# Performance work log

Hardware: AMD Instinct MI355X
Metric: run time of the kernel (lower is better)

## Reference

```python
import jax, jax.numpy as jnp
import numpy as np

N = 256          # batch size
C = 100          # nb_classes
D = 512          # sz_embed
SCALE = 3.0
EPS = 1e-12      # F.normalize eps
M = N * (N - 1) // 2  # number of (i<j) candidate pairs


def l2norm(x):
    # matches F.normalize(p=2, dim=-1) with eps=1e-12
    return x / jnp.maximum(jnp.linalg.norm(x, axis=-1, keepdims=True), EPS)


def dist_block(A, B):
    # squared euclidean distance block of pairwise_distance(cat([A,B]))[0][:len(A), len(A):]
    # (off-diagonal block, so the eye-masking in the original is a no-op; negatives zeroed)
    d = (A * A).sum(-1, keepdims=True) + (B * B).sum(-1)[None, :] - 2.0 * (A @ B.T)
    return jnp.maximum(d, 0.0)


def setup_inputs() -> dict:
    key = jax.random.key(0)
    k1, k2, k3 = jax.random.split(key, 3)
    X = jax.random.normal(k1, (N, D), dtype=jnp.float32)
    proxies = jax.random.normal(k2, (C, D), dtype=jnp.float32) / 8.0
    T = jax.random.randint(k3, (N,), 0, C)
    indices = jnp.arange(N)  # unused by forward, kept for signature fidelity
    return {"X": X, "proxies": proxies, "T": T, "indices": indices}


def reference(X, proxies, T, indices):
    Pn = SCALE * l2norm(proxies)           # (C, D)
    Xn = SCALE * l2norm(X)                 # (N, D)
    IP = Xn @ Pn.T                         # (N, C) inner-product block

    # --- intercls_mixup (method=1, uncertainty-guided lambdas) ---
    # all i<j pairs; same-class pairs are masked out (original skips them in a Python loop)
    i1, i2 = jnp.triu_indices(N, k=1)      # (M,), (M,)
    diff = T[i1] != T[i2]                  # (M,) valid cross-class pairs
    c1, c2 = T[i1], T[i2]

    X1P1 = jnp.clip(IP[i1, c1], -1.0, 1.0)
    X1P2 = jnp.clip(IP[i1, c2], -1.0, 1.0)
    X2P1 = jnp.clip(IP[i2, c1], -1.0, 1.0)
    X2P2 = jnp.clip(IP[i2, c2], -1.0, 1.0)
    lam = jnp.clip((X2P2 - X2P1) / (X2P2 - X2P1 + X1P1 - X1P2), 0.3, 0.7)
    lam = jnp.where(diff, lam, 0.5)        # neutralize masked (same-class) pairs

    virt = lam[:, None] * Xn[i1] + (1.0 - lam[:, None]) * Xn[i2]  # (M, D)
    virt = l2norm(virt)

    # --- proxy-NCA loss over real + virtual samples ---
    Xall = jnp.concatenate([Xn, SCALE * virt], axis=0)            # (N+M, D)
    Dall = dist_block(Xall, Pn)                                   # (N+M, C)
    logsm = jax.nn.log_softmax(-Dall, axis=-1)

    loss_real = -logsm[jnp.arange(N), T]                          # one-hot targets
    lv = logsm[N:]                                                # (M, C)
    rows = jnp.arange(M)
    # virtual soft targets: lam*onehot(c1) + (1-lam)*onehot(c2)
    loss_virt = -(lam * lv[rows, c1] + (1.0 - lam) * lv[rows, c2])

    total = loss_real.sum() + jnp.sum(jnp.where(diff, loss_virt, 0.0))
    count = N + diff.sum()
    return total / count
```

## Files before the change

kernel.cpp:

```cpp
#include <hip/hip_runtime.h>
#include <hip/hip_bf16.h>
#include <math.h>

#define N_ 256
#define C_ 100
#define D_ 512
#define ST 368
#define NTILE 23
#define NWTILE 529
#define LOG2E 1.44269504088896f

typedef __attribute__((ext_vector_type(8))) short short8;
typedef __attribute__((ext_vector_type(4))) float floatx4;

__device__ inline float waveReduceSum(float v) {
    #pragma unroll
    for (int off = 32; off > 0; off >>= 1) v += __shfl_xor(v, off, 64);
    return v;
}
__device__ inline float clip1(float x) { return fminf(fmaxf(x, -1.0f), 1.0f); }

__device__ inline short8 cvt8(float4 a, float4 b) {
    union { __hip_bfloat16 h[8]; short8 s; } u;
    u.h[0] = __float2bfloat16(a.x); u.h[1] = __float2bfloat16(a.y);
    u.h[2] = __float2bfloat16(a.z); u.h[3] = __float2bfloat16(a.w);
    u.h[4] = __float2bfloat16(b.x); u.h[5] = __float2bfloat16(b.y);
    u.h[6] = __float2bfloat16(b.z); u.h[7] = __float2bfloat16(b.w);
    return u.s;
}

__global__ void gemm_kernel(const float* __restrict__ X,
                            const float* __restrict__ P,
                            float* __restrict__ G,
                            float* __restrict__ rn) {
    int wid = blockIdx.x * 4 + (threadIdx.x >> 6);
    if (wid >= NWTILE) return;
    int lane = threadIdx.x & 63;
    int r = lane & 15, quad = lane >> 4;
    int tm = wid / NTILE, tn = wid - tm * NTILE;
    int ra = tm * 16 + r; if (ra >= 356) ra = 0;
    int rb = tn * 16 + r; if (rb >= 356) rb = 0;
    const float* arow = (ra < N_) ? (X + (size_t)ra * D_) : (P + (size_t)(ra - N_) * D_);
    const float* brow = (rb < N_) ? (X + (size_t)rb * D_) : (P + (size_t)(rb - N_) * D_);
    floatx4 acc = {0.0f, 0.0f, 0.0f, 0.0f};
    #pragma unroll
    for (int kc = 0; kc < D_; kc += 32) {
        const float4* ap = (const float4*)(arow + kc + quad * 8);
        const float4* bp = (const float4*)(brow + kc + quad * 8);
        short8 av = cvt8(ap[0], ap[1]);
        short8 bv = cvt8(bp[0], bp[1]);
        acc = __builtin_amdgcn_mfma_f32_16x16x32_bf16(av, bv, acc, 0, 0, 0);
    }
    int row0 = tm * 16 + quad * 4, col = tn * 16 + r;
    #pragma unroll
    for (int i = 0; i < 4; ++i)
        G[(size_t)(row0 + i) * ST + col] = acc[i];
    if (tm == tn && (r >> 2) == quad) {
        float d = acc[r & 3];
        rn[tm * 16 + r] = 3.0f * rsqrtf(fmaxf(d, 1e-24f));
    }
}

__global__ __launch_bounds__(512)
void pair_real_kernel(const float* __restrict__ G,
                      const float* __restrict__ rn,
                      const int* __restrict__ T,
                      float* __restrict__ out) {
    __shared__ int hist[C_];
    __shared__ float s2[8], ssum[8];
    int t = threadIdx.x;
    int w = t >> 6, lane = t & 63;

    if (t < C_) hist[t] = 0;
    __syncthreads();
    if (t < N_) atomicAdd(&hist[T[t]], 1);
    __syncthreads();
    float same = 0.0f;
    if (t < C_) { float n = (float)hist[t]; same = 0.5f * n * (n - 1.0f); }
    float rs = waveReduceSum(same);
    if (lane == 0) s2[w] = rs;
    __syncthreads();
    float cnt = 256.0f + 32640.0f;
    #pragma unroll
    for (int k = 0; k < 8; ++k) cnt -= s2[k];

    int i1 = blockIdx.x;
    int i2 = t >> 1;
    int p  = t & 1;
    bool diag = (i2 == i1);
    int t1 = T[i1], t2 = T[i2];
    bool act = diag || ((i2 > i1) && (t2 != t1));
    const float* sp = rn + 256;
    float contrib = 0.0f;

    if (__ballot(act)) {
        if (act) {
            float s1 = rn[i1], sc2 = rn[i2];
            const float* row1 = G + (size_t)i1 * ST + 256;
            const float* row2 = G + (size_t)i2 * ST + 256;
            float ip1t1 = row1[t1] * s1 * sp[t1];
            float ip1t2 = row1[t2] * s1 * sp[t2];
            float ip2t1 = row2[t1] * sc2 * sp[t1];
            float ip2t2 = row2[t2] * sc2 * sp[t2];
            float X1P1 = clip1(ip1t1), X1P2 = clip1(ip1t2);
            float X2P1 = clip1(ip2t1), X2P2 = clip1(ip2t2);
            float num = X2P2 - X2P1;
            float den = num + X1P1 - X1P2;
            float lam = fminf(fmaxf(num / den, 0.3f), 0.7f);
            if (diag) lam = 1.0f;
            float oml = 1.0f - lam;
            float g = G[(size_t)i1 * ST + i2] * s1 * sc2;
            float wn2 = 9.0f * (lam * lam + oml * oml) + 2.0f * lam * oml * g;
            float ss2 = 6.0f * rsqrtf(fmaxf(wn2, 1e-24f));
            float la = ss2 * lam * s1 * LOG2E, lb = ss2 * oml * sc2 * LOG2E;
            float sm0 = 0.0f, sm1 = 0.0f, sm2 = 0.0f, sm3 = 0.0f;
            #pragma unroll 4
            for (int c = 4 * p; c < C_; c += 8) {
                float4 a1 = *(const float4*)(row1 + c);
                float4 a2 = *(const float4*)(row2 + c);
                float4 s4 = *(const float4*)(sp + c);
                sm0 += exp2f(s4.x * (la * a1.x + lb * a2.x));
                sm1 += exp2f(s4.y * (la * a1.y + lb * a2.y));
                sm2 += exp2f(s4.z * (la * a1.z + lb * a2.z));
                sm3 += exp2f(s4.w * (la * a1.w + lb * a2.w));
            }
            float sm = (sm0 + sm1) + (sm2 + sm3);
            sm += __shfl_xor(sm, 1, 64);
            if (p == 0) {
                float LSE = logf(sm);
                float ec1 = ss2 * (lam * ip1t1 + oml * ip2t1);
                float ec2 = ss2 * (lam * ip1t2 + oml * ip2t2);
                contrib = LSE - lam * ec1 - oml * ec2;
            }
        }
    }
    contrib = waveReduceSum(contrib);
    if (lane == 0) ssum[w] = contrib;
    __syncthreads();
    if (t == 0) {
        float bs = 0.0f;
        #pragma unroll
        for (int k = 0; k < 8; ++k) bs += ssum[k];
        atomicAdd(out, bs / cnt);
    }
}

extern "C" void kernel_launch(void* const* d_in, const int* in_sizes, int n_in,
                              void* d_out, int out_size, void* d_ws, size_t ws_size,
                              hipStream_t stream) {
    const float* X = (const float*)d_in[0];
    const float* P = (const float*)d_in[1];
    const int*   T = (const int*)d_in[2];
    float* ws = (float*)d_ws;
    float* G  = ws;
    float* rn = ws + 135424;
    float* out = (float*)d_out;

    gemm_kernel<<<133, 256, 0, stream>>>(X, P, G, rn);
    pair_real_kernel<<<N_, 512, 0, stream>>>(G, rn, T, out);
}
```

Baseline: 73.42 us.

## Fuse GEMM and pair-loss into single kernel with per-block LDS proxy slab

Replaces the separate GEMM and pair-loss kernels with one fused kernel. Each block converts the proxies to bf16 in LDS, computes inner products for its 129 circularly-indexed rows with MFMA, and evaluates the pair losses directly from LDS. This removes the global intermediate and one launch and balances pairs across blocks. The cost is redundant proxy conversion and GEMM work in every block, and large LDS use that limits occupancy to one block per CU.

Measured after the change: 83.69 us. +14.0%, slower.

```diff
diff --git a/kernel.cpp b/kernel.cpp
--- a/kernel.cpp
+++ b/kernel.cpp
@@ -5,10 +5,19 @@
 #define N_ 256
 #define C_ 100
 #define D_ 512
-#define ST 368
-#define NTILE 23
-#define NWTILE 529
 #define LOG2E 1.44269504088896f
+#define XPST 102
+#define PBROWB 64
+#define PBSLAB 6464
+
+#define OFF_PB    0
+#define OFF_XPN   103424
+#define OFF_TL    156056
+#define OFF_HIST  157080
+#define OFF_SPS   157480
+#define OFF_RED   157928
+#define OFF_S2    157960
+#define LDS_TOTAL 157992
 
 typedef __attribute__((ext_vector_type(8))) short short8;
 typedef __attribute__((ext_vector_type(4))) float floatx4;
@@ -29,119 +38,171 @@
     return u.s;
 }
 
-__global__ void gemm_kernel(const float* __restrict__ X,
-                            const float* __restrict__ P,
-                            float* __restrict__ G,
-                            float* __restrict__ rn) {
-    int wid = blockIdx.x * 4 + (threadIdx.x >> 6);
-    if (wid >= NWTILE) return;
-    int lane = threadIdx.x & 63;
-    int r = lane & 15, quad = lane >> 4;
-    int tm = wid / NTILE, tn = wid - tm * NTILE;
-    int ra = tm * 16 + r; if (ra >= 356) ra = 0;
-    int rb = tn * 16 + r; if (rb >= 356) rb = 0;
-    const float* arow = (ra < N_) ? (X + (size_t)ra * D_) : (P + (size_t)(ra - N_) * D_);
-    const float* brow = (rb < N_) ? (X + (size_t)rb * D_) : (P + (size_t)(rb - N_) * D_);
-    floatx4 acc = {0.0f, 0.0f, 0.0f, 0.0f};
-    #pragma unroll
-    for (int kc = 0; kc < D_; kc += 32) {
-        const float4* ap = (const float4*)(arow + kc + quad * 8);
-        const float4* bp = (const float4*)(brow + kc + quad * 8);
-        short8 av = cvt8(ap[0], ap[1]);
-        short8 bv = cvt8(bp[0], bp[1]);
-        acc = __builtin_amdgcn_mfma_f32_16x16x32_bf16(av, bv, acc, 0, 0, 0);
-    }
-    int row0 = tm * 16 + quad * 4, col = tn * 16 + r;
-    #pragma unroll
-    for (int i = 0; i < 4; ++i)
-        G[(size_t)(row0 + i) * ST + col] = acc[i];
-    if (tm == tn && (r >> 2) == quad) {
-        float d = acc[r & 3];
-        rn[tm * 16 + r] = 3.0f * rsqrtf(fmaxf(d, 1e-24f));
-    }
-}
-
 __global__ __launch_bounds__(512)
-void pair_real_kernel(const float* __restrict__ G,
-                      const float* __restrict__ rn,
-                      const int* __restrict__ T,
-                      float* __restrict__ out) {
-    __shared__ int hist[C_];
-    __shared__ float s2[8], ssum[8];
+void fused_kernel(const float* __restrict__ X, const float* __restrict__ P,
+                  const int* __restrict__ T, float* __restrict__ out) {
+    extern __shared__ char smem[];
+    short* Pb   = (short*)(smem + OFF_PB);
+    float* XPn  = (float*)(smem + OFF_XPN);
+    int*   Tl   = (int*)(smem + OFF_TL);
+    int*   hist = (int*)(smem + OFF_HIST);
+    float* sps  = (float*)(smem + OFF_SPS);
+    float* red  = (float*)(smem + OFF_RED);
+    float* s2   = (float*)(smem + OFF_S2);
+
     int t = threadIdx.x;
     int w = t >> 6, lane = t & 63;
+    int b = blockIdx.x;
 
     if (t < C_) hist[t] = 0;
+    if (t < N_) Tl[t] = T[t];
+
+    for (int j = 0; j < 13; ++j) {
+        int ch = t + 512 * j;
+        float s8 = 0.0f;
+        if (ch < 6400) {
+            int pr = ch >> 6, cl = ch & 63;
+            const float4* pp = (const float4*)(P + (size_t)pr * D_ + cl * 8);
+            float4 a = pp[0], c4 = pp[1];
+            s8 = a.x*a.x + a.y*a.y + a.z*a.z + a.w*a.w
+               + c4.x*c4.x + c4.y*c4.y + c4.z*c4.z + c4.w*c4.w;
+            short8 v = cvt8(a, c4);
+            *(short8*)((char*)Pb + (cl >> 2) * PBSLAB + pr * PBROWB + (cl & 3) * 16) = v;
+        }
+        float rs = waveReduceSum(s8);
+        int pr0 = w + 8 * j;
+        if (lane == 0 && pr0 < C_) sps[pr0] = 3.0f * rsqrtf(fmaxf(rs, 1e-24f));
+    }
+    if (t < 64) {
+        const float4* xp = (const float4*)(X + (size_t)b * D_ + t * 8);
+        short8 v = cvt8(xp[0], xp[1]);
+        *(short8*)((char*)Pb + (t >> 2) * PBSLAB + 100 * PBROWB + (t & 3) * 16) = v;
+    }
+    float sxb;
+    {
+        const float4* xp = (const float4*)(X + (size_t)b * D_ + lane * 8);
+        float4 a = xp[0], c4 = xp[1];
+        float xb2 = a.x*a.x + a.y*a.y + a.z*a.z + a.w*a.w
+                  + c4.x*c4.x + c4.y*c4.y + c4.z*c4.z + c4.w*c4.w;
+        xb2 = waveReduceSum(xb2);
+        sxb = 3.0f * rsqrtf(fmaxf(xb2, 1e-24f));
+    }
+
     __syncthreads();
-    if (t < N_) atomicAdd(&hist[T[t]], 1);
+
+    if (t < N_) atomicAdd(&hist[Tl[t]], 1);
+
+    int r = lane & 15, quad = lane >> 4;
+    int boff[7];
+    #pragma unroll
+    for (int tn = 0; tn < 7; ++tn) {
+        int cb = tn * 16 + r;
+        if (cb > 100) cb = 0;
+        boff[tn] = cb * PBROWB + quad * 16;
+    }
+    for (int rt = w; rt < 9; rt += 8) {
+        int lr0 = rt * 16;
+        int ra = (b + lr0 + r) & 255;
+        const float* arow = X + (size_t)ra * D_;
+        floatx4 acc[7];
+        #pragma unroll
+        for (int tn = 0; tn < 7; ++tn) acc[tn] = (floatx4){0.f, 0.f, 0.f, 0.f};
+        float nrm = 0.0f;
+        #pragma unroll 4
+        for (int kc = 0; kc < D_; kc += 32) {
+            const float4* ap = (const float4*)(arow + kc + quad * 8);
+            float4 a0 = ap[0], a1 = ap[1];
+            nrm += a0.x*a0.x + a0.y*a0.y + a0.z*a0.z + a0.w*a0.w
+                 + a1.x*a1.x + a1.y*a1.y + a1.z*a1.z + a1.w*a1.w;
+            short8 av = cvt8(a0, a1);
+            const char* sl = (const char*)Pb + (kc >> 5) * PBSLAB;
+            #pragma unroll
+            for (int tn = 0; tn < 7; ++tn) {
+                short8 bv = *(const short8*)(sl + boff[tn]);
+                acc[tn] = __builtin_amdgcn_mfma_f32_16x16x32_bf16(av, bv, acc[tn], 0, 0, 0);
+            }
+        }
+        nrm += __shfl_xor(nrm, 16, 64);
+        nrm += __shfl_xor(nrm, 32, 64);
+        float sxa = 3.0f * rsqrtf(fmaxf(nrm, 1e-24f));
+        float sxr[4];
+        #pragma unroll
+        for (int i = 0; i < 4; ++i) sxr[i] = __shfl(sxa, quad * 4 + i, 64);
+        #pragma unroll
+        for (int tn = 0; tn < 7; ++tn) {
+            int colw = tn * 16 + r;
+            if (colw <= 100) {
+                float cs = (colw < 100) ? sps[colw] : sxb;
+                #pragma unroll
+                for (int i = 0; i < 4; ++i) {
+                    int lr = lr0 + quad * 4 + i;
+                    if (lr <= 128) XPn[lr * XPST + colw] = acc[tn][i] * sxr[i] * cs;
+                }
+            }
+        }
+    }
     __syncthreads();
+
     float same = 0.0f;
     if (t < C_) { float n = (float)hist[t]; same = 0.5f * n * (n - 1.0f); }
-    float rs = waveReduceSum(same);
-    if (lane == 0) s2[w] = rs;
-    __syncthreads();
-    float cnt = 256.0f + 32640.0f;
-    #pragma unroll
-    for (int k = 0; k < 8; ++k) cnt -= s2[k];
-
-    int i1 = blockIdx.x;
-    int i2 = t >> 1;
-    int p  = t & 1;
-    bool diag = (i2 == i1);
-    int t1 = T[i1], t2 = T[i2];
-    bool act = diag || ((i2 > i1) && (t2 != t1));
-    const float* sp = rn + 256;
+    float rsame = waveReduceSum(same);
+    if (lane == 0) s2[w] = rsame;
+
+    int m = t >> 1, p = t & 1;
+    bool diag = (m == 128);
+    int d = m + 1;
+    int lr2 = diag ? 0 : d;
+    int i2 = diag ? b : ((b + d) & 255);
+    bool isPair = (m < 127) || (m == 127 && b < 128);
+    int t1 = Tl[b], t2 = Tl[i2];
+    bool act = diag || (isPair && (t2 != t1));
     float contrib = 0.0f;
-
     if (__ballot(act)) {
         if (act) {
-            float s1 = rn[i1], sc2 = rn[i2];
-            const float* row1 = G + (size_t)i1 * ST + 256;
-            const float* row2 = G + (size_t)i2 * ST + 256;
-            float ip1t1 = row1[t1] * s1 * sp[t1];
-            float ip1t2 = row1[t2] * s1 * sp[t2];
-            float ip2t1 = row2[t1] * sc2 * sp[t1];
-            float ip2t2 = row2[t2] * sc2 * sp[t2];
-            float X1P1 = clip1(ip1t1), X1P2 = clip1(ip1t2);
-            float X2P1 = clip1(ip2t1), X2P2 = clip1(ip2t2);
+            const float* rowA = XPn;
+            const float* rowB = XPn + lr2 * XPST;
+            float ip11 = rowA[t1], ip12 = rowA[t2];
+            float ip21 = rowB[t1], ip22 = rowB[t2];
+            float X1P1 = clip1(ip11), X1P2 = clip1(ip12);
+            float X2P1 = clip1(ip21), X2P2 = clip1(ip22);
             float num = X2P2 - X2P1;
             float den = num + X1P1 - X1P2;
             float lam = fminf(fmaxf(num / den, 0.3f), 0.7f);
             if (diag) lam = 1.0f;
             float oml = 1.0f - lam;
-            float g = G[(size_t)i1 * ST + i2] * s1 * sc2;
+            float g = rowB[100];
             float wn2 = 9.0f * (lam * lam + oml * oml) + 2.0f * lam * oml * g;
             float ss2 = 6.0f * rsqrtf(fmaxf(wn2, 1e-24f));
-            float la = ss2 * lam * s1 * LOG2E, lb = ss2 * oml * sc2 * LOG2E;
-            float sm0 = 0.0f, sm1 = 0.0f, sm2 = 0.0f, sm3 = 0.0f;
+            float la = ss2 * lam * LOG2E, lb = ss2 * oml * LOG2E;
+            float sm0 = 0, sm1 = 0, sm2 = 0, sm3 = 0;
             #pragma unroll 4
-            for (int c = 4 * p; c < C_; c += 8) {
-                float4 a1 = *(const float4*)(row1 + c);
-                float4 a2 = *(const float4*)(row2 + c);
-                float4 s4 = *(const float4*)(sp + c);
-                sm0 += exp2f(s4.x * (la * a1.x + lb * a2.x));
-                sm1 += exp2f(s4.y * (la * a1.y + lb * a2.y));
-                sm2 += exp2f(s4.z * (la * a1.z + lb * a2.z));
-                sm3 += exp2f(s4.w * (la * a1.w + lb * a2.w));
+            for (int k = 0; k < 13; ++k) {
+                int c = 4 * p + 8 * k;
+                if (c < C_) {
+                    sm0 += exp2f(la * rowA[c]     + lb * rowB[c]);
+                    sm1 += exp2f(la * rowA[c + 1] + lb * rowB[c + 1]);
+                    sm2 += exp2f(la * rowA[c + 2] + lb * rowB[c + 2]);
+                    sm3 += exp2f(la * rowA[c + 3] + lb * rowB[c + 3]);
+                }
             }
             float sm = (sm0 + sm1) + (sm2 + sm3);
             sm += __shfl_xor(sm, 1, 64);
             if (p == 0) {
                 float LSE = logf(sm);
-                float ec1 = ss2 * (lam * ip1t1 + oml * ip2t1);
-                float ec2 = ss2 * (lam * ip1t2 + oml * ip2t2);
+                float ec1 = ss2 * (lam * ip11 + oml * ip21);
+                float ec2 = ss2 * (lam * ip12 + oml * ip22);
                 contrib = LSE - lam * ec1 - oml * ec2;
             }
         }
     }
     contrib = waveReduceSum(contrib);
-    if (lane == 0) ssum[w] = contrib;
+    if (lane == 0) red[w] = contrib;
     __syncthreads();
     if (t == 0) {
-        float bs = 0.0f;
-        #pragma unroll
-        for (int k = 0; k < 8; ++k) bs += ssum[k];
-        atomicAdd(out, bs / cnt);
+        float bs = 0.0f, sc = 0.0f;
+        #pragma unroll
+        for (int k = 0; k < 8; ++k) { bs += red[k]; sc += s2[k]; }
+        atomicAdd(out, bs / (32896.0f - sc));
     }
 }
 
@@ -151,11 +212,13 @@
     const float* X = (const float*)d_in[0];
     const float* P = (const float*)d_in[1];
     const int*   T = (const int*)d_in[2];
-    float* ws = (float*)d_ws;
-    float* G  = ws;
-    float* rn = ws + 135424;
     float* out = (float*)d_out;
 
-    gemm_kernel<<<133, 256, 0, stream>>>(X, P, G, rn);
-    pair_real_kernel<<<N_, 512, 0, stream>>>(G, rn, T, out);
-}
+    static bool init = false;
+    if (!init) {
+        hipFuncSetAttribute((const void*)fused_kernel,
+                            hipFuncAttributeMaxDynamicSharedMemorySize, LDS_TOTAL);
+        init = true;
+    }
+    fused_kernel<<<N_, 512, LDS_TOTAL, stream>>>(X, P, T, out);
+}
```

## Rebalance pair kernel with circulant pairing and shared-memory staged rows

Applied to the files above, without the earlier changes.

Replaces the triangular per-row pair assignment (row i1 handles i2>i1, so block work is badly imbalanced) with a circulant scheme: each of 512 blocks handles row b paired with 64 cyclic offsets, giving every block equal work. The G rows for the partner samples, proxy scales, norms and labels are staged into LDS so the logsumexp loop reads shared memory, and 8 lanes split each pair's 100 classes. The histogram-based pair count is folded into the final reduction. The cost is extra LDS staging per block and more complex index logic for the half-offset (dd==128) case.

Result: slower. 77.54 us (+5.6%).

```diff
diff --git a/kernel.cpp b/kernel.cpp
--- a/kernel.cpp
+++ b/kernel.cpp
@@ -62,86 +62,104 @@
 }
 
 __global__ __launch_bounds__(512)
-void pair_real_kernel(const float* __restrict__ G,
-                      const float* __restrict__ rn,
-                      const int* __restrict__ T,
-                      float* __restrict__ out) {
-    __shared__ int hist[C_];
-    __shared__ float s2[8], ssum[8];
+void pair_kernel(const float* __restrict__ G, const float* __restrict__ rn,
+                 const int* __restrict__ T, float* __restrict__ out) {
+    __shared__ __attribute__((aligned(16))) float XPl[64 * 104];
+    __shared__ __attribute__((aligned(16))) float al[104];
+    __shared__ __attribute__((aligned(16))) float sps[104];
+    __shared__ float gl[256];
+    __shared__ float sxs[256];
+    __shared__ int   Tl[256];
+    __shared__ int   hist[104];
+    __shared__ float red[8];
+
     int t = threadIdx.x;
     int w = t >> 6, lane = t & 63;
+    int bh = blockIdx.x;
+    int b = bh & 255, h = bh >> 8;
+    int base = h * 64 + 1;
 
-    if (t < C_) hist[t] = 0;
+    if (t < 104) { hist[t] = 0; sps[t] = (t < C_) ? rn[256 + t] : 0.0f; }
+    if (t < 256) { sxs[t] = rn[t]; Tl[t] = T[t]; gl[t] = G[(size_t)b * ST + t]; }
+    if (t < C_)  al[t] = G[(size_t)b * ST + 256 + t];
+    #pragma unroll
+    for (int it = 0; it < 4; ++it) {
+        int id = t + 512 * it;
+        if (id < 1600) {
+            int row = id / 25, c4 = id - row * 25;
+            int gr = (b + base + row) & 255;
+            *(float4*)&XPl[row * 104 + c4 * 4] =
+                *(const float4*)(G + (size_t)gr * ST + 256 + c4 * 4);
+        }
+    }
     __syncthreads();
-    if (t < N_) atomicAdd(&hist[T[t]], 1);
-    __syncthreads();
-    float same = 0.0f;
-    if (t < C_) { float n = (float)hist[t]; same = 0.5f * n * (n - 1.0f); }
-    float rs = waveReduceSum(same);
-    if (lane == 0) s2[w] = rs;
-    __syncthreads();
-    float cnt = 256.0f + 32640.0f;
-    #pragma unroll
-    for (int k = 0; k < 8; ++k) cnt -= s2[k];
+    if (t < 256) atomicAdd(&hist[Tl[t]], 1);
 
-    int i1 = blockIdx.x;
-    int i2 = t >> 1;
-    int p  = t & 1;
-    bool diag = (i2 == i1);
-    int t1 = T[i1], t2 = T[i2];
-    bool act = diag || ((i2 > i1) && (t2 != t1));
-    const float* sp = rn + 256;
+    int m = t >> 3, q = t & 7;
+    int t1 = Tl[b];
+    float s1 = sxs[b];
     float contrib = 0.0f;
-
-    if (__ballot(act)) {
-        if (act) {
-            float s1 = rn[i1], sc2 = rn[i2];
-            const float* row1 = G + (size_t)i1 * ST + 256;
-            const float* row2 = G + (size_t)i2 * ST + 256;
-            float ip1t1 = row1[t1] * s1 * sp[t1];
-            float ip1t2 = row1[t2] * s1 * sp[t2];
-            float ip2t1 = row2[t1] * sc2 * sp[t1];
-            float ip2t2 = row2[t2] * sc2 * sp[t2];
-            float X1P1 = clip1(ip1t1), X1P2 = clip1(ip1t2);
-            float X2P1 = clip1(ip2t1), X2P2 = clip1(ip2t2);
-            float num = X2P2 - X2P1;
-            float den = num + X1P1 - X1P2;
-            float lam = fminf(fmaxf(num / den, 0.3f), 0.7f);
-            if (diag) lam = 1.0f;
-            float oml = 1.0f - lam;
-            float g = G[(size_t)i1 * ST + i2] * s1 * sc2;
-            float wn2 = 9.0f * (lam * lam + oml * oml) + 2.0f * lam * oml * g;
-            float ss2 = 6.0f * rsqrtf(fmaxf(wn2, 1e-24f));
-            float la = ss2 * lam * s1 * LOG2E, lb = ss2 * oml * sc2 * LOG2E;
-            float sm0 = 0.0f, sm1 = 0.0f, sm2 = 0.0f, sm3 = 0.0f;
-            #pragma unroll 4
-            for (int c = 4 * p; c < C_; c += 8) {
-                float4 a1 = *(const float4*)(row1 + c);
-                float4 a2 = *(const float4*)(row2 + c);
-                float4 s4 = *(const float4*)(sp + c);
-                sm0 += exp2f(s4.x * (la * a1.x + lb * a2.x));
-                sm1 += exp2f(s4.y * (la * a1.y + lb * a2.y));
-                sm2 += exp2f(s4.z * (la * a1.z + lb * a2.z));
-                sm3 += exp2f(s4.w * (la * a1.w + lb * a2.w));
-            }
-            float sm = (sm0 + sm1) + (sm2 + sm3);
-            sm += __shfl_xor(sm, 1, 64);
-            if (p == 0) {
-                float LSE = logf(sm);
-                float ec1 = ss2 * (lam * ip1t1 + oml * ip2t1);
-                float ec2 = ss2 * (lam * ip1t2 + oml * ip2t2);
-                contrib = LSE - lam * ec1 - oml * ec2;
+    int nit = (h == 0 && m == 0) ? 2 : 1;
+    for (int it = 0; it < nit; ++it) {
+        bool isdiag = (it == 1);
+        int dd = base + m;
+        int i2 = isdiag ? b : ((b + dd) & 255);
+        int t2 = Tl[i2];
+        bool act = isdiag || ((t2 != t1) && (dd < 128 || b < 128));
+        if (!act) continue;
+        const float* rowB = isdiag ? al : &XPl[m * 104];
+        float sc2 = sxs[i2];
+        float ip11 = al[t1] * s1 * sps[t1];
+        float ip12 = al[t2] * s1 * sps[t2];
+        float ip21 = rowB[t1] * sc2 * sps[t1];
+        float ip22 = rowB[t2] * sc2 * sps[t2];
+        float X1P1 = clip1(ip11), X1P2 = clip1(ip12);
+        float X2P1 = clip1(ip21), X2P2 = clip1(ip22);
+        float num = X2P2 - X2P1;
+        float den = num + X1P1 - X1P2;
+        float lam = fminf(fmaxf(num / den, 0.3f), 0.7f);
+        if (isdiag) lam = 1.0f;
+        float oml = 1.0f - lam;
+        float g = gl[i2] * s1 * sc2;
+        float wn2 = 9.0f * (lam * lam + oml * oml) + 2.0f * lam * oml * g;
+        float ss2 = 6.0f * rsqrtf(fmaxf(wn2, 1e-24f));
+        float la = ss2 * lam * s1 * LOG2E, lb = ss2 * oml * sc2 * LOG2E;
+        float sm = 0.0f;
+        #pragma unroll
+        for (int k = 0; k < 4; ++k) {
+            int c = q * 4 + 32 * k;
+            if (c < C_) {
+                float4 a1 = *(const float4*)&al[c];
+                float4 a2 = *(const float4*)&rowB[c];
+                float4 s4 = *(const float4*)&sps[c];
+                sm += exp2f(s4.x * (la * a1.x + lb * a2.x));
+                sm += exp2f(s4.y * (la * a1.y + lb * a2.y));
+                sm += exp2f(s4.z * (la * a1.z + lb * a2.z));
+                sm += exp2f(s4.w * (la * a1.w + lb * a2.w));
             }
         }
+        sm += __shfl_xor(sm, 1, 64);
+        sm += __shfl_xor(sm, 2, 64);
+        sm += __shfl_xor(sm, 4, 64);
+        if (q == 0) {
+            float LSE = logf(sm);
+            float ec1 = ss2 * (lam * ip11 + oml * ip21);
+            float ec2 = ss2 * (lam * ip12 + oml * ip22);
+            contrib += LSE - lam * ec1 - oml * ec2;
+        }
     }
-    contrib = waveReduceSum(contrib);
-    if (lane == 0) ssum[w] = contrib;
+    float rsum = waveReduceSum(contrib);
+    if (lane == 0) red[w] = rsum;
     __syncthreads();
-    if (t == 0) {
-        float bs = 0.0f;
-        #pragma unroll
-        for (int k = 0; k < 8; ++k) bs += ssum[k];
-        atomicAdd(out, bs / cnt);
+
+    if (w == 0) {
+        float same = 0.0f;
+        { float n = (float)hist[lane]; same = 0.5f * n * (n - 1.0f); }
+        if (lane + 64 < C_) { float n = (float)hist[lane + 64]; same += 0.5f * n * (n - 1.0f); }
+        float bs = (lane < 8) ? red[lane] : 0.0f;
+        same = waveReduceSum(same);
+        bs = waveReduceSum(bs);
+        if (lane == 0) atomicAdd(out, bs / (32896.0f - same));
     }
 }
 
@@ -157,5 +175,5 @@
     float* out = (float*)d_out;
 
     gemm_kernel<<<133, 256, 0, stream>>>(X, P, G, rn);
-    pair_real_kernel<<<N_, 512, 0, stream>>>(G, rn, T, out);
+    pair_kernel<<<512, 512, 0, stream>>>(G, rn, T, out);
 }
```
